# Kernel optimization log

Measured on AMD Instinct MI355X. Metric: run time of the kernel, lower is better.

Reference implementation:

```python
import jax, jax.numpy as jnp
import numpy as np
import math

D_MODEL = 512
HEADS = 8
GRID_COUNT = 40000
MAX_LEN = 5000


def _positional_embedding(d_model, max_len=MAX_LEN):
    pe = np.zeros((max_len, d_model), dtype=np.float32)
    position = np.arange(max_len, dtype=np.float32)[:, None]
    div_term = np.exp(np.arange(0, d_model, 2, dtype=np.float32) * -(math.log(10000.0) / d_model))
    pe[:, 0::2] = np.sin(position * div_term)
    pe[:, 1::2] = np.cos(position * div_term)
    return jnp.asarray(pe)  # [max_len, d_model]


def _mha(q, k, v, wq, bq, wk, bk, wv, bv, heads):
    # Faithful to SelfAttention: no 1/sqrt(d_k) scaling in the original.
    B, Sq, D = q.shape
    Sk = k.shape[1]
    dh = D // heads
    Q = (q @ wq.T + bq).reshape(B, Sq, heads, dh)
    K = (k @ wk.T + bk).reshape(B, Sk, heads, dh)
    V = (v @ wv.T + bv).reshape(B, Sk, heads, dh)
    attn = jax.nn.softmax(jnp.einsum('bqhd,bkhd->bhqk', Q, K), axis=-1)
    out = jnp.einsum('bhqk,bkhd->bqhd', attn, V)
    return out.reshape(B, Sq, D)


def setup_inputs() -> dict:
    key = jax.random.key(0)
    ks = jax.random.split(key, 20)
    B, S_CURR, S_HIST, N_MASK = 32, 128, 256, 16
    s = 1.0 / math.sqrt(D_MODEL)

    def lin(k):
        kw, kb = jax.random.split(k)
        w = jax.random.uniform(kw, (D_MODEL, D_MODEL), jnp.float32, -s, s)
        b = jax.random.uniform(kb, (D_MODEL,), jnp.float32, -s, s)
        return w, b

    h_wq, h_bq = lin(ks[0]); h_wk, h_bk = lin(ks[1]); h_wv, h_bv = lin(ks[2])
    c_wq, c_bq = lin(ks[3]); c_wk, c_bk = lin(ks[4]); c_wv, c_bv = lin(ks[5])
    x_wq, x_bq = lin(ks[6]); x_wk, x_bk = lin(ks[7]); x_wv, x_bv = lin(ks[8])
    t2_w, t2_b = lin(ks[9])
    emb = jax.random.normal(ks[10], (GRID_COUNT, D_MODEL), jnp.float32)

    return {
        'hist_traj_grid': jax.random.randint(ks[11], (B, S_HIST), 0, GRID_COUNT),
        'userId': jax.random.randint(ks[12], (B,), 0, 1000),
        'mask_pos': jax.random.randint(ks[13], (B, N_MASK), 0, S_CURR),
        'mask_curr_traj_grid': jax.random.randint(ks[14], (B, S_CURR), 0, GRID_COUNT),
        'aggregator_hist_traj_grid': jax.random.randint(ks[15], (B, S_HIST), 0, GRID_COUNT),
        'emb': emb,
        'h_wq': h_wq, 'h_bq': h_bq, 'h_wk': h_wk, 'h_bk': h_bk, 'h_wv': h_wv, 'h_bv': h_bv,
        'c_wq': c_wq, 'c_bq': c_bq, 'c_wk': c_wk, 'c_bk': c_bk, 'c_wv': c_wv, 'c_bv': c_bv,
        'x_wq': x_wq, 'x_bq': x_bq, 'x_wk': x_wk, 'x_bk': x_bk, 'x_wv': x_wv, 'x_bv': x_bv,
        't2_w': t2_w, 't2_b': t2_b,
    }


def reference(hist_traj_grid, userId, mask_pos, mask_curr_traj_grid, aggregator_hist_traj_grid,
              emb,
              h_wq, h_bq, h_wk, h_bk, h_wv, h_bv,
              c_wq, c_bq, c_wk, c_bk, c_wv, c_bv,
              x_wq, x_bq, x_wk, x_bk, x_wv, x_bv,
              t2_w, t2_b):
    pe = _positional_embedding(D_MODEL)
    hist = emb[aggregator_hist_traj_grid]          # [B, S_hist, D]
    curr = emb[mask_curr_traj_grid]                # [B, S_curr, D]
    hist = hist + pe[None, :hist.shape[1]]
    curr = curr + pe[None, :curr.shape[1]]

    hist = _mha(hist, hist, hist, h_wq, h_bq, h_wk, h_bk, h_wv, h_bv, HEADS)
    curr = _mha(curr, curr, curr, c_wq, c_bq, c_wk, c_bk, c_wv, c_bv, HEADS)
    _cross = _mha(curr, hist, hist, x_wq, x_bq, x_wk, x_bk, x_wv, x_bv, HEADS)
    # NOTE: original overwrites liner_transform output with liner_transform2(tanh(curr)),
    # so cross-attention output and liner_transform do not affect the result.
    hyb = jnp.tanh(curr) @ t2_w.T + t2_b           # [B, S_curr, D]

    # index_select of flattened [B*S, D] at mask_pos + b*S == take_along_axis over seq dim
    gathered = jnp.take_along_axis(hyb, mask_pos[:, :, None], axis=1)  # [B, n_mask, D]
    gathered = gathered.reshape(-1, D_MODEL)

    candidate = emb[2:]                            # [vocab-2, D]
    scores = gathered @ candidate.T                # [B*n_mask, vocab-2]
    return jax.nn.log_softmax(scores, axis=-1)
```

## Files before the change

kernel.cpp:

```cpp
#include <hip/hip_runtime.h>
#include <hip/hip_bf16.h>
#include <math.h>
#include <float.h>

#define B       32
#define S_CURR  128
#define D       512
#define H       8
#define DH      64
#define NM      16
#define NCAND   39998
#define MG      (B * NM)
#define SCLD    40064
#define NT      313

typedef __bf16 bf16x8_t __attribute__((ext_vector_type(8)));
typedef __bf16 bf16x4_t __attribute__((ext_vector_type(4)));
typedef float  f32x4_t  __attribute__((ext_vector_type(4)));

typedef __attribute__((address_space(3))) unsigned int lds_u32_t;
typedef const __attribute__((address_space(1))) unsigned int gbl_u32_t;

__device__ __forceinline__ void async16(const void* g, void* l) {
    __builtin_amdgcn_global_load_lds((gbl_u32_t*)g, (lds_u32_t*)l, 16, 0, 0);
}

__global__ __launch_bounds__(256) void prep_kernel(
    const float* __restrict__ emb,
    const float* __restrict__ wq, const float* __restrict__ wk,
    const float* __restrict__ wv, const float* __restrict__ t2w,
    __bf16* __restrict__ embB, __bf16* __restrict__ wqB, __bf16* __restrict__ wkB,
    __bf16* __restrict__ wvB, __bf16* __restrict__ t2wB,
    const int* __restrict__ curr_idx, __bf16* __restrict__ currB,
    const int* __restrict__ mask_pos, int* __restrict__ qidx)
{
    int bx = blockIdx.x;
    if (bx < 10512) {
        const float* src; __bf16* dst; size_t n, base;
        if (bx < 10000) {
            src = emb + 2 * D; dst = embB; n = (size_t)NCAND * D; base = (size_t)bx * 2048;
        } else {
            int w = (bx - 10000) >> 7;
            base = (size_t)((bx - 10000) & 127) * 2048;
            n = (size_t)D * D;
            src = (w == 0) ? wq : (w == 1) ? wk : (w == 2) ? wv : t2w;
            dst = (w == 0) ? wqB : (w == 1) ? wkB : (w == 2) ? wvB : t2wB;
        }
        size_t i = base + (size_t)threadIdx.x * 8;
        if (i >= n) return;
        float4 a = *(const float4*)(src + i);
        float4 b = *(const float4*)(src + i + 4);
        bf16x8_t v;
        v[0] = (__bf16)a.x; v[1] = (__bf16)a.y; v[2] = (__bf16)a.z; v[3] = (__bf16)a.w;
        v[4] = (__bf16)b.x; v[5] = (__bf16)b.y; v[6] = (__bf16)b.z; v[7] = (__bf16)b.w;
        *(bf16x8_t*)(dst + i) = v;
        return;
    }
    if (bx == 14608) {
        int r = threadIdx.x;
        qidx[r] = (r >> 4) * S_CURR + mask_pos[r];
        r += 256;
        qidx[r] = (r >> 4) * S_CURR + mask_pos[r];
        return;
    }
    int bs = bx - 10512;
    int s = bs & (S_CURR - 1);
    int g = curr_idx[bs];
    const float* e = emb + (size_t)g * D;
    __bf16* o = currB + (size_t)bs * D;
    int d = threadIdx.x * 2;
    float div = expf(-(float)d * (9.210340371976184f / 512.0f));
    float ang = (float)s * div;
    o[d]     = (__bf16)(e[d]     + sinf(ang));
    o[d + 1] = (__bf16)(e[d + 1] + cosf(ang));
}

__global__ __launch_bounds__(256) void gemm_bf(
    const __bf16* __restrict__ A,
    const __bf16* __restrict__ W0, const float* __restrict__ b0, __bf16* __restrict__ C0,
    const __bf16* __restrict__ W1, const float* __restrict__ b1, __bf16* __restrict__ C1,
    const __bf16* __restrict__ W2, const float* __restrict__ b2, __bf16* __restrict__ C2,
    const int* __restrict__ rowidx)
{
    const int z = blockIdx.z;
    if (z == 2 && blockIdx.x >= 4) return;
    const __bf16* W = (z == 0) ? W0 : (z == 1) ? W1 : W2;
    const float* bias = (z == 0) ? b0 : (z == 1) ? b1 : b2;
    __bf16* C = (z == 0) ? C0 : (z == 1) ? C1 : C2;

    __shared__ __bf16 As[2][128 * 64];
    __shared__ __bf16 Bs[2][128 * 64];

    const int tid = threadIdx.x, lane = tid & 63, wave = tid >> 6;
    const int wy = wave >> 1, wx = wave & 1;
    const int m0 = blockIdx.x * 128, n0 = blockIdx.y * 128;
    const int lrow = lane >> 3;
    const int lcol = (((lane & 7) ^ lrow) & 7) * 8;

    const __bf16* aptr[4]; const __bf16* bptr[4];
#pragma unroll
    for (int i = 0; i < 4; ++i) {
        int chunk = wave * 4 + i;
        int ar = m0 + chunk * 8 + lrow;
        if (z == 2) ar = rowidx[ar];
        aptr[i] = A + (size_t)ar * 512 + lcol;
        bptr[i] = W + (size_t)(n0 + chunk * 8 + lrow) * 512 + lcol;
    }

    f32x4_t acc[4][4];
#pragma unroll
    for (int i = 0; i < 4; ++i)
#pragma unroll
        for (int j = 0; j < 4; ++j) acc[i][j] = (f32x4_t){0.f, 0.f, 0.f, 0.f};

    const int l7 = lane & 7, quad = lane >> 4, c16 = lane & 15;

#pragma unroll
    for (int i = 0; i < 4; ++i) {
        int chunk = wave * 4 + i;
        async16(aptr[i], &As[0][chunk * 512]);
        async16(bptr[i], &Bs[0][chunk * 512]);
    }

#pragma unroll
    for (int t = 0; t < 8; ++t) {
        const int cur = t & 1;
        if (t < 7) {
            const int kk = (t + 1) * 64;
#pragma unroll
            for (int i = 0; i < 4; ++i) {
                int chunk = wave * 4 + i;
                async16(aptr[i] + kk, &As[cur ^ 1][chunk * 512]);
                async16(bptr[i] + kk, &Bs[cur ^ 1][chunk * 512]);
            }
            asm volatile("s_waitcnt vmcnt(8)" ::: "memory");
        } else {
            asm volatile("s_waitcnt vmcnt(0)" ::: "memory");
        }
        __builtin_amdgcn_s_barrier();
#pragma unroll
        for (int kb = 0; kb < 2; ++kb) {
            const int goff = (((kb * 4 + quad) ^ l7)) * 8;
            bf16x8_t af[4], bfv[4];
#pragma unroll
            for (int i = 0; i < 4; ++i)
                af[i] = *(const bf16x8_t*)&As[cur][(wy * 64 + i * 16 + c16) * 64 + goff];
#pragma unroll
            for (int j = 0; j < 4; ++j)
                bfv[j] = *(const bf16x8_t*)&Bs[cur][(wx * 64 + j * 16 + c16) * 64 + goff];
#pragma unroll
            for (int i = 0; i < 4; ++i)
#pragma unroll
                for (int j = 0; j < 4; ++j)
                    acc[i][j] = __builtin_amdgcn_mfma_f32_16x16x32_bf16(
                        bfv[j], af[i], acc[i][j], 0, 0, 0);
        }
        asm volatile("s_waitcnt lgkmcnt(0)" ::: "memory");
        __builtin_amdgcn_s_barrier();
    }

#pragma unroll
    for (int i = 0; i < 4; ++i) {
        const int row = m0 + wy * 64 + i * 16 + c16;
#pragma unroll
        for (int j = 0; j < 4; ++j) {
            const int colb = n0 + wx * 64 + j * 16 + quad * 4;
            float4 bv = *(const float4*)&bias[colb];
            bf16x4_t o;
            o[0] = (__bf16)(acc[i][j][0] + bv.x);
            o[1] = (__bf16)(acc[i][j][1] + bv.y);
            o[2] = (__bf16)(acc[i][j][2] + bv.z);
            o[3] = (__bf16)(acc[i][j][3] + bv.w);
            *(bf16x4_t*)&C[(size_t)row * 512 + colb] = o;
        }
    }
}

__global__ __launch_bounds__(256) void gemm_scores(
    const __bf16* __restrict__ A,
    const __bf16* __restrict__ Bm,
    __bf16* __restrict__ scB,
    float* __restrict__ pmax, float* __restrict__ psum)
{
    const int bid = blockIdx.x;
    const int xcd = bid & 7, k = bid >> 3;
    const int nt = xcd * 40 + (k >> 2);
    if (nt >= NT) return;
    const int m0 = (k & 3) * 128, n0 = nt * 128;

    __shared__ __bf16 As[2][128 * 64];
    __shared__ __bf16 Bs[2][128 * 64];
    __shared__ float redm[2][128], reds[2][128];

    const int tid = threadIdx.x, lane = tid & 63, wave = tid >> 6;
    const int wy = wave >> 1, wx = wave & 1;
    const int lrow = lane >> 3;
    const int lcol = (((lane & 7) ^ lrow) & 7) * 8;

    const __bf16* aptr[4]; const __bf16* bptr[4];
#pragma unroll
    for (int i = 0; i < 4; ++i) {
        int chunk = wave * 4 + i;
        aptr[i] = A + (size_t)(m0 + chunk * 8 + lrow) * 512 + lcol;
        bptr[i] = Bm + (size_t)(n0 + chunk * 8 + lrow) * 512 + lcol;
    }

    f32x4_t acc[4][4];
#pragma unroll
    for (int i = 0; i < 4; ++i)
#pragma unroll
        for (int j = 0; j < 4; ++j) acc[i][j] = (f32x4_t){0.f, 0.f, 0.f, 0.f};

    const int l7 = lane & 7, quad = lane >> 4, c16 = lane & 15;

#pragma unroll
    for (int i = 0; i < 4; ++i) {
        int chunk = wave * 4 + i;
        async16(aptr[i], &As[0][chunk * 512]);
        async16(bptr[i], &Bs[0][chunk * 512]);
    }

#pragma unroll
    for (int t = 0; t < 8; ++t) {
        const int cur = t & 1;
        if (t < 7) {
            const int kk = (t + 1) * 64;
#pragma unroll
            for (int i = 0; i < 4; ++i) {
                int chunk = wave * 4 + i;
                async16(aptr[i] + kk, &As[cur ^ 1][chunk * 512]);
                async16(bptr[i] + kk, &Bs[cur ^ 1][chunk * 512]);
            }
            asm volatile("s_waitcnt vmcnt(8)" ::: "memory");
        } else {
            asm volatile("s_waitcnt vmcnt(0)" ::: "memory");
        }
        __builtin_amdgcn_s_barrier();
#pragma unroll
        for (int kb = 0; kb < 2; ++kb) {
            const int goff = (((kb * 4 + quad) ^ l7)) * 8;
            bf16x8_t af[4], bfv[4];
#pragma unroll
            for (int i = 0; i < 4; ++i)
                af[i] = *(const bf16x8_t*)&As[cur][(wy * 64 + i * 16 + c16) * 64 + goff];
#pragma unroll
            for (int j = 0; j < 4; ++j)
                bfv[j] = *(const bf16x8_t*)&Bs[cur][(wx * 64 + j * 16 + c16) * 64 + goff];
#pragma unroll
            for (int i = 0; i < 4; ++i)
#pragma unroll
                for (int j = 0; j < 4; ++j)
                    acc[i][j] = __builtin_amdgcn_mfma_f32_16x16x32_bf16(
                        bfv[j], af[i], acc[i][j], 0, 0, 0);
        }
        asm volatile("s_waitcnt lgkmcnt(0)" ::: "memory");
        __builtin_amdgcn_s_barrier();
    }

    const bool tailb = (n0 + 128 > NCAND);
#pragma unroll
    for (int i = 0; i < 4; ++i) {
        const int lrw = wy * 64 + i * 16 + c16;
        const size_t rowbase = (size_t)(m0 + lrw) * SCLD;
        float vs[4][4];
        float vmax = -FLT_MAX;
        float ssum = 0.f;
        if (!tailb) {
#pragma unroll
            for (int j = 0; j < 4; ++j) {
                const int nb = n0 + wx * 64 + j * 16 + quad * 4;
                bf16x4_t o;
#pragma unroll
                for (int rr = 0; rr < 4; ++rr) {
                    __bf16 xb = (__bf16)acc[i][j][rr];
                    o[rr] = xb;
                    float xr = (float)xb;
                    vs[j][rr] = xr;
                    vmax = fmaxf(vmax, xr);
                }
                *(bf16x4_t*)&scB[rowbase + nb] = o;
            }
#pragma unroll
            for (int j = 0; j < 4; ++j)
#pragma unroll
                for (int rr = 0; rr < 4; ++rr)
                    ssum += __expf(vs[j][rr] - vmax);
        } else {
            for (int j = 0; j < 4; ++j) {
                const int nb = n0 + wx * 64 + j * 16 + quad * 4;
                for (int rr = 0; rr < 4; ++rr) {
                    const int n = nb + rr;
                    __bf16 xb = (__bf16)acc[i][j][rr];
                    float xr = (float)xb;
                    if (n < NCAND) {
                        scB[rowbase + n] = xb;
                        vs[j][rr] = xr;
                        vmax = fmaxf(vmax, xr);
                    } else vs[j][rr] = -FLT_MAX;
                }
            }
            for (int j = 0; j < 4; ++j)
                for (int rr = 0; rr < 4; ++rr)
                    ssum += (vs[j][rr] > -FLT_MAX) ? __expf(vs[j][rr] - vmax) : 0.f;
        }
#pragma unroll
        for (int mk = 16; mk < 64; mk <<= 1) {
            float om = __shfl_xor(vmax, mk);
            float os = __shfl_xor(ssum, mk);
            float mm = fmaxf(vmax, om);
            ssum = ssum * __expf(vmax - mm) + os * __expf(om - mm);
            vmax = mm;
        }
        if (quad == 0) { redm[wx][lrw] = vmax; reds[wx][lrw] = ssum; }
    }
    __syncthreads();
    if (tid < 128) {
        float ma = redm[0][tid], sa = reds[0][tid];
        float mb = redm[1][tid], sb = reds[1][tid];
        float mm = fmaxf(ma, mb);
        float ss = sa * __expf(ma - mm) + sb * __expf(mb - mm);
        pmax[(size_t)(m0 + tid) * NT + nt] = mm;
        psum[(size_t)(m0 + tid) * NT + nt] = ss;
    }
}

#define KPAD 72
__global__ __launch_bounds__(256) void attn_kernel(const __bf16* __restrict__ Qg,
                                                   const __bf16* __restrict__ K,
                                                   const __bf16* __restrict__ V,
                                                   __bf16* __restrict__ attnB) {
    const int b = blockIdx.x, h = blockIdx.y, t = threadIdx.x;
    __shared__ __bf16 Ks[128 * KPAD];
    __shared__ __bf16 Vs[128 * KPAD];
    __shared__ float  Qs[16 * 68];
    __shared__ float  P[16 * 130];

    for (int i = t; i < 1024; i += 256) {
        int row = i >> 3, cg = (i & 7) * 8;
        size_t gsrc = ((size_t)(b * S_CURR + row)) * D + h * DH + cg;
        *(bf16x8_t*)&Ks[row * KPAD + cg] = *(const bf16x8_t*)&K[gsrc];
        *(bf16x8_t*)&Vs[row * KPAD + cg] = *(const bf16x8_t*)&V[gsrc];
    }
    if (t < 128) {
        int q = t >> 3, cg = (t & 7) * 8;
        bf16x8_t qv = *(const bf16x8_t*)&Qg[((size_t)(b * NM + q)) * D + h * DH + cg];
#pragma unroll
        for (int u = 0; u < 8; ++u) Qs[q * 68 + cg + u] = (float)qv[u];
    }
    __syncthreads();

    const int q = t >> 4, i = t & 15;
    float sv[8];
    float lmax = -FLT_MAX;
#pragma unroll
    for (int z = 0; z < 8; ++z) {
        int kk = i + z * 16;
        float s = 0.f;
#pragma unroll
        for (int d0 = 0; d0 < DH; d0 += 8) {
            bf16x8_t kv = *(const bf16x8_t*)&Ks[kk * KPAD + d0];
#pragma unroll
            for (int u = 0; u < 8; ++u) s += Qs[q * 68 + d0 + u] * (float)kv[u];
        }
        sv[z] = s; lmax = fmaxf(lmax, s);
    }
#pragma unroll
    for (int mk = 1; mk < 16; mk <<= 1) lmax = fmaxf(lmax, __shfl_xor(lmax, mk));
    float lsum = 0.f;
#pragma unroll
    for (int z = 0; z < 8; ++z) {
        float e = __expf(sv[z] - lmax);
        P[q * 130 + i + z * 16] = e;
        lsum += e;
    }
#pragma unroll
    for (int mk = 1; mk < 16; mk <<= 1) lsum += __shfl_xor(lsum, mk);
    const float inv = 1.0f / lsum;

    const int d = i * 4;
    float a0 = 0.f, a1 = 0.f, a2 = 0.f, a3 = 0.f;
    for (int kk = 0; kk < 128; ++kk) {
        float p = P[q * 130 + kk];
        bf16x4_t vv = *(const bf16x4_t*)&Vs[kk * KPAD + d];
        a0 += p * (float)vv[0]; a1 += p * (float)vv[1];
        a2 += p * (float)vv[2]; a3 += p * (float)vv[3];
    }
    __bf16* o = attnB + ((size_t)(b * NM + q)) * D + h * DH + d;
    o[0] = (__bf16)tanhf(a0 * inv); o[1] = (__bf16)tanhf(a1 * inv);
    o[2] = (__bf16)tanhf(a2 * inv); o[3] = (__bf16)tanhf(a3 * inv);
}

__global__ __launch_bounds__(256) void lse_reduce(const float* __restrict__ pmax,
                                                  const float* __restrict__ psum,
                                                  float* __restrict__ lse) {
    int row = blockIdx.x, t = threadIdx.x;
    float m = -FLT_MAX, s = 0.f;
    for (int i = t; i < NT; i += 256) {
        float om = pmax[(size_t)row * NT + i];
        float os = psum[(size_t)row * NT + i];
        float mm = fmaxf(m, om);
        s = s * __expf(m - mm) + os * __expf(om - mm);
        m = mm;
    }
    __shared__ float ms[256], ss[256];
    ms[t] = m; ss[t] = s;
    __syncthreads();
    for (int off = 128; off > 0; off >>= 1) {
        if (t < off) {
            float m1 = ms[t], s1 = ss[t], m2 = ms[t + off], s2 = ss[t + off];
            float mm = fmaxf(m1, m2);
            ms[t] = mm;
            ss[t] = s1 * __expf(m1 - mm) + s2 * __expf(m2 - mm);
        }
        __syncthreads();
    }
    if (t == 0) lse[row] = ms[0] + logf(ss[0]);
}

__global__ __launch_bounds__(256) void final_out(const __bf16* __restrict__ scB,
                                                 const float* __restrict__ lse,
                                                 float* __restrict__ out) {
    int row = blockIdx.y;
    int c0 = (blockIdx.x * 256 + threadIdx.x) * 8;
    if (c0 >= NCAND) return;
    float l = lse[row];
    bf16x8_t v = *(const bf16x8_t*)(scB + (size_t)row * SCLD + c0);
    float* o = out + (size_t)row * NCAND + c0;
    if (c0 + 8 <= NCAND) {
        *(float2*)(o)     = make_float2((float)v[0] - l, (float)v[1] - l);
        *(float2*)(o + 2) = make_float2((float)v[2] - l, (float)v[3] - l);
        *(float2*)(o + 4) = make_float2((float)v[4] - l, (float)v[5] - l);
        *(float2*)(o + 6) = make_float2((float)v[6] - l, (float)v[7] - l);
    } else {
        for (int k2 = 0; k2 < NCAND - c0; ++k2) o[k2] = (float)v[k2] - l;
    }
}

extern "C" void kernel_launch(void* const* d_in, const int* in_sizes, int n_in,
                              void* d_out, int out_size, void* d_ws, size_t ws_size,
                              hipStream_t stream) {
    const int*   mask_pos = (const int*)d_in[2];
    const int*   curr_idx = (const int*)d_in[3];
    const float* emb      = (const float*)d_in[5];
    const float* c_wq = (const float*)d_in[12];
    const float* c_bq = (const float*)d_in[13];
    const float* c_wk = (const float*)d_in[14];
    const float* c_bk = (const float*)d_in[15];
    const float* c_wv = (const float*)d_in[16];
    const float* c_bv = (const float*)d_in[17];
    const float* t2_w = (const float*)d_in[24];
    const float* t2_b = (const float*)d_in[25];
    float* out = (float*)d_out;

    char* w = (char*)d_ws;
    __bf16* embB  = (__bf16*)w;
    __bf16* scB   = (__bf16*)(w + 41025536);
    __bf16* currB = scB;
    __bf16* Kf    = (__bf16*)(w + 41025536 + 4194304);
    __bf16* Vf    = (__bf16*)(w + 41025536 + 8388608);
    __bf16* Qg    = (__bf16*)(w + 41025536 + 12582912);
    __bf16* attnB = (__bf16*)(w + 41025536 + 13107200);
    __bf16* wqB   = (__bf16*)(w + 41025536 + 13631488);
    __bf16* wkB   = (__bf16*)(w + 41025536 + 14155776);
    __bf16* wvB   = (__bf16*)(w + 41025536 + 14680064);
    __bf16* t2wB  = (__bf16*)(w + 41025536 + 15204352);
    int*    qidx  = (int*)   (w + 41025536 + 15728640);
    __bf16* gatheredB = (__bf16*)(w + 82051072);
    float*  pmax  = (float*)(w + 82575360);
    float*  psum  = (float*)(w + 83216384);
    float*  lse   = (float*)(w + 83857408);

    hipLaunchKernelGGL(prep_kernel, dim3(14609), dim3(256), 0, stream,
                       emb, c_wq, c_wk, c_wv, t2_w, embB, wqB, wkB, wvB, t2wB,
                       curr_idx, currB, mask_pos, qidx);
    hipLaunchKernelGGL(gemm_bf, dim3(32, 4, 3), dim3(256), 0, stream,
                       currB, wkB, c_bk, Kf, wvB, c_bv, Vf, wqB, c_bq, Qg, qidx);
    hipLaunchKernelGGL(attn_kernel, dim3(B, H), dim3(256), 0, stream,
                       Qg, Kf, Vf, attnB);
    hipLaunchKernelGGL(gemm_bf, dim3(4, 4, 1), dim3(256), 0, stream,
                       attnB, t2wB, t2_b, gatheredB,
                       t2wB, t2_b, gatheredB, t2wB, t2_b, gatheredB,
                       (const int*)nullptr);
    hipLaunchKernelGGL(gemm_scores, dim3(1280), dim3(256), 0, stream,
                       gatheredB, embB, scB, pmax, psum);
    hipLaunchKernelGGL(lse_reduce, dim3(MG), dim3(256), 0, stream, pmax, psum, lse);
    hipLaunchKernelGGL(final_out, dim3(20, MG), dim3(256), 0, stream, scB, lse, out);
}
```

Baseline: 292.5 us.

## Load A fragments directly to registers and triple-buffer B tiles in scores GEMM

The scores GEMM no longer stages the A operand through LDS. Each wave now reads its A fragments straight from global memory into registers, and the freed LDS holds a third B buffer so B tiles are prefetched two k-steps ahead. This is meant to cut LDS traffic and space, and to hide more global-memory latency behind the MFMA work. In exchange, the two waves sharing the same A rows now fetch them separately from global/L2, and the hand-written vmcnt waits have to account for the extra register loads in the queue.

```diff
diff --git a/kernel.cpp b/kernel.cpp
--- a/kernel.cpp
+++ b/kernel.cpp
@@ -188,22 +188,24 @@
     if (nt >= NT) return;
     const int m0 = (k & 3) * 128, n0 = nt * 128;
 
-    __shared__ __bf16 As[2][128 * 64];
-    __shared__ __bf16 Bs[2][128 * 64];
+    __shared__ __bf16 Bs[3][128 * 64];
     __shared__ float redm[2][128], reds[2][128];
 
     const int tid = threadIdx.x, lane = tid & 63, wave = tid >> 6;
     const int wy = wave >> 1, wx = wave & 1;
     const int lrow = lane >> 3;
     const int lcol = (((lane & 7) ^ lrow) & 7) * 8;
-
-    const __bf16* aptr[4]; const __bf16* bptr[4];
-#pragma unroll
-    for (int i = 0; i < 4; ++i) {
-        int chunk = wave * 4 + i;
-        aptr[i] = A + (size_t)(m0 + chunk * 8 + lrow) * 512 + lcol;
-        bptr[i] = Bm + (size_t)(n0 + chunk * 8 + lrow) * 512 + lcol;
-    }
+    const int l7 = lane & 7, quad = lane >> 4, c16 = lane & 15;
+
+    const __bf16* bptr[4];
+#pragma unroll
+    for (int i = 0; i < 4; ++i)
+        bptr[i] = Bm + (size_t)(n0 + (wave * 4 + i) * 8 + lrow) * 512 + lcol;
+
+    const __bf16* arow[4];
+#pragma unroll
+    for (int i = 0; i < 4; ++i)
+        arow[i] = A + (size_t)(m0 + wy * 64 + i * 16 + c16) * 512 + quad * 8;
 
     f32x4_t acc[4][4];
 #pragma unroll
@@ -211,27 +213,29 @@
 #pragma unroll
         for (int j = 0; j < 4; ++j) acc[i][j] = (f32x4_t){0.f, 0.f, 0.f, 0.f};
 
-    const int l7 = lane & 7, quad = lane >> 4, c16 = lane & 15;
-
-#pragma unroll
-    for (int i = 0; i < 4; ++i) {
-        int chunk = wave * 4 + i;
-        async16(aptr[i], &As[0][chunk * 512]);
-        async16(bptr[i], &Bs[0][chunk * 512]);
-    }
+#pragma unroll
+    for (int i = 0; i < 4; ++i)
+        async16(bptr[i], &Bs[0][(wave * 4 + i) * 512]);
+#pragma unroll
+    for (int i = 0; i < 4; ++i)
+        async16(bptr[i] + 64, &Bs[1][(wave * 4 + i) * 512]);
 
 #pragma unroll
     for (int t = 0; t < 8; ++t) {
-        const int cur = t & 1;
-        if (t < 7) {
-            const int kk = (t + 1) * 64;
-#pragma unroll
-            for (int i = 0; i < 4; ++i) {
-                int chunk = wave * 4 + i;
-                async16(aptr[i] + kk, &As[cur ^ 1][chunk * 512]);
-                async16(bptr[i] + kk, &Bs[cur ^ 1][chunk * 512]);
-            }
+        const int cur = t % 3;
+        bf16x8_t af[4][2];
+#pragma unroll
+        for (int i = 0; i < 4; ++i)
+#pragma unroll
+            for (int kb = 0; kb < 2; ++kb)
+                af[i][kb] = *(const bf16x8_t*)(arow[i] + t * 64 + kb * 32);
+        if (t < 6) {
+#pragma unroll
+            for (int i = 0; i < 4; ++i)
+                async16(bptr[i] + (t + 2) * 64, &Bs[(t + 2) % 3][(wave * 4 + i) * 512]);
             asm volatile("s_waitcnt vmcnt(8)" ::: "memory");
+        } else if (t == 6) {
+            asm volatile("s_waitcnt vmcnt(4)" ::: "memory");
         } else {
             asm volatile("s_waitcnt vmcnt(0)" ::: "memory");
         }
@@ -239,10 +243,7 @@
 #pragma unroll
         for (int kb = 0; kb < 2; ++kb) {
             const int goff = (((kb * 4 + quad) ^ l7)) * 8;
-            bf16x8_t af[4], bfv[4];
-#pragma unroll
-            for (int i = 0; i < 4; ++i)
-                af[i] = *(const bf16x8_t*)&As[cur][(wy * 64 + i * 16 + c16) * 64 + goff];
+            bf16x8_t bfv[4];
 #pragma unroll
             for (int j = 0; j < 4; ++j)
                 bfv[j] = *(const bf16x8_t*)&Bs[cur][(wx * 64 + j * 16 + c16) * 64 + goff];
@@ -251,7 +252,7 @@
 #pragma unroll
                 for (int j = 0; j < 4; ++j)
                     acc[i][j] = __builtin_amdgcn_mfma_f32_16x16x32_bf16(
-                        bfv[j], af[i], acc[i][j], 0, 0, 0);
+                        bfv[j], af[i][kb], acc[i][j], 0, 0, 0);
         }
         asm volatile("s_waitcnt lgkmcnt(0)" ::: "memory");
         __builtin_amdgcn_s_barrier();
```

Measured after the change: 303.9 us. 3.9% more time.
